# Optimization experiments

Hardware: AMD Instinct MI355X
Metric: run time of the kernel (lower is better)

## Reference

```python
import jax, jax.numpy as jnp
from jax import lax
import numpy as np

ANCHOR_LENGTHS = (2.0, 4.0, 6.0, 9.0, 13.0, 18.0)  # A = 6


def make_anchors_1d(Lf, anchor_lengths):
    # anchors on the feature axis: [Lf*A, 2] (start, end)
    al = jnp.asarray(anchor_lengths, dtype=jnp.float32)          # [A]
    centers = jnp.arange(Lf, dtype=jnp.float32) + 0.5            # [Lf]
    start = centers[:, None] - 0.5 * al[None, :]                 # [Lf, A]
    end = centers[:, None] + 0.5 * al[None, :]                   # [Lf, A]
    return jnp.stack([start, end], axis=-1).reshape(Lf * al.shape[0], 2)


def setup_inputs() -> dict:
    key = jax.random.key(0)
    ks = jax.random.split(key, 4)
    B, C, Lf, A = 4, 512, 8192, len(ANCHOR_LENGTHS)
    feat = jax.random.normal(ks[0], (B, C, Lf), dtype=jnp.float32)
    conv_w = jax.random.normal(ks[1], (C, C, 3), dtype=jnp.float32) * 0.02   # OIW
    conv_b = jnp.zeros((C,), dtype=jnp.float32)
    obj_w = jax.random.normal(ks[2], (A, C, 1), dtype=jnp.float32) * 0.02
    obj_b = jnp.zeros((A,), dtype=jnp.float32)
    reg_w = jax.random.normal(ks[3], (A * 2, C, 1), dtype=jnp.float32) * 0.02
    reg_b = jnp.zeros((A * 2,), dtype=jnp.float32)
    return {"feat": feat, "conv_w": conv_w, "conv_b": conv_b,
            "obj_w": obj_w, "obj_b": obj_b, "reg_w": reg_w, "reg_b": reg_b}


def reference(feat, conv_w, conv_b, obj_w, obj_b, reg_w, reg_b):
    B, C, Lf = feat.shape
    A = obj_w.shape[0]
    # 3x1 conv, padding=1 -> SAME; layout N C W / O I W
    h = lax.conv_general_dilated(feat, conv_w, window_strides=(1,),
                                 padding="SAME",
                                 dimension_numbers=("NCH", "OIH", "NCH"))
    h = jax.nn.relu(h + conv_b[None, :, None])                   # [B, C, Lf]
    # 1x1 conv heads expressed as channel contractions
    obj = jnp.einsum("bcl,ac->bal", h, obj_w[:, :, 0]) + obj_b[None, :, None]   # [B, A, Lf]
    reg = jnp.einsum("bcl,ac->bal", h, reg_w[:, :, 0]) + reg_b[None, :, None]   # [B, 2A, Lf]
    obj = obj.transpose(0, 2, 1).reshape(B, Lf * A)                              # [B, N]
    reg = reg.transpose(0, 2, 1).reshape(B, Lf, A, 2).reshape(B, Lf * A, 2)      # [B, N, 2]
    anchors = make_anchors_1d(Lf, ANCHOR_LENGTHS)                                # [N, 2]
    return obj, reg, anchors
```

## Files before the change

kernel.cpp:

```cpp
#include <hip/hip_runtime.h>
#include <stdint.h>

typedef __attribute__((ext_vector_type(8))) short short8;
typedef __attribute__((ext_vector_type(4))) float f32x4;
typedef __attribute__((ext_vector_type(4))) float float4v;
typedef __attribute__((ext_vector_type(4))) unsigned short u16x4;
typedef __attribute__((ext_vector_type(8))) unsigned short u16x8;

#define AS1 __attribute__((address_space(1)))
#define AS3 __attribute__((address_space(3)))


__device__ __forceinline__ unsigned short f2bf(float f) {
    union { float f; unsigned int u; } v; v.f = f;
    unsigned int r = v.u + 0x7fffu + ((v.u >> 16) & 1u);
    return (unsigned short)(r >> 16);
}

__constant__ float c_AL[6] = {2.f, 4.f, 6.f, 9.f, 13.f, 18.f};

__global__ __launch_bounds__(256) void prep_kernel(
    const float* __restrict__ conv_w, const float* __restrict__ obj_w,
    const float* __restrict__ reg_w, const float* __restrict__ obj_b,
    const float* __restrict__ reg_b, unsigned short* __restrict__ wAf,
    unsigned short* __restrict__ hwp, unsigned short* __restrict__ featT,
    float* __restrict__ out) {
    unsigned int idx = blockIdx.x * 256 + threadIdx.x;
    if (idx < 786432u) {
        unsigned int chunkid = idx >> 9;
        unsigned int within = idx & 511u;
        unsigned int lane = within >> 3, j = within & 7u;
        unsigned int kc = chunkid & 15u;
        unsigned int ct = chunkid >> 4;
        unsigned int t = ct % 3u, cb = ct / 3u;
        unsigned int cout = cb * 16u + (lane & 15u);
        unsigned int cin = kc * 32u + (lane >> 4) * 8u + j;
        wAf[idx] = f2bf(conv_w[(cout * 512u + cin) * 3u + t]);
    } else if (idx < 802816u) {
        unsigned int i2 = idx - 786432u;
        unsigned int j = i2 >> 9, c = i2 & 511u;
        float v = 0.f;
        if (j < 6u) v = obj_w[j * 512u + c];
        else if (j < 18u) v = reg_w[(j - 6u) * 512u + c];
        hwp[i2] = f2bf(v);
    } else if (idx < 851968u) {
        unsigned int n = idx - 802816u;
        unsigned int l = n / 6u, a = n - l * 6u;
        float ctr = (float)l + 0.5f, half = 0.5f * c_AL[a];
        float* anchors = out + 589824;
        anchors[2 * n]     = ctr - half;
        anchors[2 * n + 1] = ctr + half;
    } else if (idx < 856064u) {
        unsigned int i4 = idx - 851968u;
        unsigned int b = i4 >> 10, rem = i4 & 1023u;
        unsigned int row = (rem >> 9) ? 8193u : 0u;
        unsigned int c = rem & 511u;
        featT[((size_t)b * 8208 + row) * 512 + c] = 0;
    } else if (idx < 1052672u) {
        unsigned int i = idx - 856064u;
        out[i] = obj_b[i % 6u];
    } else if (idx < 1445888u) {
        unsigned int i = idx - 1052672u;
        out[196608u + i] = reg_b[i % 12u];
    }
}

__global__ __launch_bounds__(256) void transpose_kernel(
    const float* __restrict__ feat, unsigned short* __restrict__ featT) {
    __shared__ float tileT[64][69];
    int tid = threadIdx.x;
    int l0 = blockIdx.x * 64, c0 = blockIdx.y * 64, b = blockIdx.z;
    const float* fb = feat + ((size_t)b * 512 + c0) * 8192 + l0;
    #pragma unroll
    for (int it = 0; it < 4; ++it) {
        int slot = it * 256 + tid;
        int c = slot >> 4, l4 = (slot & 15) << 2;
        float4v v = *(const float4v*)(fb + (size_t)c * 8192 + l4);
        tileT[l4][c] = v.x; tileT[l4 + 1][c] = v.y;
        tileT[l4 + 2][c] = v.z; tileT[l4 + 3][c] = v.w;
    }
    __syncthreads();
    unsigned short* ftb = featT + ((size_t)b * 8208 + 1 + l0) * 512 + c0;
    #pragma unroll
    for (int it = 0; it < 2; ++it) {
        int slot = it * 256 + tid;
        int l = slot >> 3, c8 = (slot & 7) << 3;
        u16x8 pk;
        #pragma unroll
        for (int j = 0; j < 8; ++j) pk[j] = f2bf(tileT[l][c8 + j]);
        *(u16x8*)(ftb + (size_t)l * 512 + c8) = pk;
    }
}

__global__ __launch_bounds__(256, 3) void conv_gemm_kernel(
    const unsigned short* __restrict__ wAf,
    const unsigned short* __restrict__ featT,
    const float* __restrict__ conv_b,
    const unsigned short* __restrict__ hwp,
    float* __restrict__ out) {
    __shared__ unsigned short smem[17408];

    const int tid = threadIdx.x;
    const int wave = tid >> 6, lane = tid & 63;
    const int lq = lane >> 4, lr = lane & 15;
    const int l0 = blockIdx.x * 128;
    const int m0 = blockIdx.y * 128;
    const int b = blockIdx.z;
    const int wm = wave >> 1, wn = wave & 1;
    const unsigned short* ftb = featT + (size_t)b * 8208 * 512;

    f32x4 acc[4][4];
    #pragma unroll
    for (int i = 0; i < 4; ++i)
        #pragma unroll
        for (int j = 0; j < 4; ++j)
            acc[i][j] = (f32x4){0.f, 0.f, 0.f, 0.f};

    for (int kc = 0; kc < 16; ++kc) {
        __syncthreads();
        for (int ci = wave; ci < 33; ci += 4) {
            const unsigned short* g;
            if (ci < 24) {
                int t = ci >> 3, rb = ci & 7;
                g = wAf + ((size_t)(((m0 >> 4) + rb) * 3 + t) * 16 + kc) * 512 + lane * 8;
            } else {
                int lb = ci - 24;
                g = ftb + (size_t)(l0 + lb * 16 + lr) * 512 + kc * 32 + lq * 8;
            }
            __builtin_amdgcn_global_load_lds((const AS1 void*)g,
                                             (AS3 void*)(smem + ci * 512), 16, 0, 0);
        }
        __syncthreads();
        #pragma unroll
        for (int t = 0; t < 3; ++t) {
            short8 af[4], bf[4];
            #pragma unroll
            for (int fm = 0; fm < 4; ++fm)
                af[fm] = *(const short8*)(smem + ((t * 8 + wm * 4 + fm) << 9) + (lane << 3));
            #pragma unroll
            for (int fn = 0; fn < 4; ++fn) {
                int R = wn * 64 + fn * 16 + lr + t;
                bf[fn] = *(const short8*)(smem + ((24 + (R >> 4)) << 9) +
                                          ((((lq << 4) | (R & 15))) << 3));
            }
            #pragma unroll
            for (int fm = 0; fm < 4; ++fm)
                #pragma unroll
                for (int fn = 0; fn < 4; ++fn)
                    acc[fm][fn] = __builtin_amdgcn_mfma_f32_16x16x32_bf16(
                        af[fm], bf[fn], acc[fm][fn], 0, 0, 0);
        }
    }
    __syncthreads();
    #pragma unroll
    for (int fm = 0; fm < 4; ++fm) {
        int mb = wm * 64 + fm * 16 + lq * 4;
        float cb0 = conv_b[m0 + mb];
        float cb1 = conv_b[m0 + mb + 1];
        float cb2 = conv_b[m0 + mb + 2];
        float cb3 = conv_b[m0 + mb + 3];
        #pragma unroll
        for (int fn = 0; fn < 4; ++fn) {
            int n = wn * 64 + fn * 16 + lr;
            f32x4 v = acc[fm][fn];
            u16x4 pk;
            pk.x = f2bf(fmaxf(v.x + cb0, 0.f));
            pk.y = f2bf(fmaxf(v.y + cb1, 0.f));
            pk.z = f2bf(fmaxf(v.z + cb2, 0.f));
            pk.w = f2bf(fmaxf(v.w + cb3, 0.f));
            *(u16x4*)(smem + n * 136 + mb) = pk;
        }
    }
    __syncthreads();
    f32x4 hacc[2][2];
    #pragma unroll
    for (int i = 0; i < 2; ++i) {
        hacc[i][0] = (f32x4){0.f, 0.f, 0.f, 0.f};
        hacc[i][1] = (f32x4){0.f, 0.f, 0.f, 0.f};
    }
    const int lbase = wave * 32;
    for (int kk = 0; kk < 4; ++kk) {
        short8 ha[2], hb2[2];
        #pragma unroll
        for (int fm2 = 0; fm2 < 2; ++fm2)
            ha[fm2] = *(const short8*)(smem + (lbase + fm2 * 16 + lr) * 136 + kk * 32 + lq * 8);
        #pragma unroll
        for (int fn = 0; fn < 2; ++fn)
            hb2[fn] = *(const short8*)(hwp + (size_t)(fn * 16 + lr) * 512 + m0 + kk * 32 + lq * 8);
        #pragma unroll
        for (int fm2 = 0; fm2 < 2; ++fm2)
            #pragma unroll
            for (int fn = 0; fn < 2; ++fn)
                hacc[fm2][fn] = __builtin_amdgcn_mfma_f32_16x16x32_bf16(
                    ha[fm2], hb2[fn], hacc[fm2][fn], 0, 0, 0);
    }
    float* outObj = out + (size_t)b * 49152;
    float* outReg = out + 196608 + (size_t)b * 98304;
    #pragma unroll
    for (int fn = 0; fn < 2; ++fn) {
        int j = fn * 16 + lr;
        if (j >= 18) continue;
        #pragma unroll
        for (int fm2 = 0; fm2 < 2; ++fm2)
            #pragma unroll
            for (int r = 0; r < 4; ++r) {
                int l = l0 + lbase + fm2 * 16 + lq * 4 + r;
                float v = hacc[fm2][fn][r];
                if (j < 6) atomicAdd(&outObj[l * 6 + j], v);
                else atomicAdd(&outReg[l * 12 + (j - 6)], v);
            }
    }
}

extern "C" void kernel_launch(void* const* d_in, const int* in_sizes, int n_in,
                              void* d_out, int out_size, void* d_ws, size_t ws_size,
                              hipStream_t stream) {
    const float* feat   = (const float*)d_in[0];
    const float* conv_w = (const float*)d_in[1];
    const float* conv_b = (const float*)d_in[2];
    const float* obj_w  = (const float*)d_in[3];
    const float* obj_b  = (const float*)d_in[4];
    const float* reg_w  = (const float*)d_in[5];
    const float* reg_b  = (const float*)d_in[6];
    float* out = (float*)d_out;
    char* ws = (char*)d_ws;
    unsigned short* wAf   = (unsigned short*)(ws);
    unsigned short* hwp   = (unsigned short*)(ws + 1572864);
    unsigned short* featT = (unsigned short*)(ws + 1605632);

    prep_kernel<<<dim3(5648), dim3(256), 0, stream>>>(conv_w, obj_w, reg_w, obj_b,
                                                      reg_b, wAf, hwp, featT, out);
    transpose_kernel<<<dim3(128, 8, 4), dim3(256), 0, stream>>>(feat, featT);
    conv_gemm_kernel<<<dim3(64, 4, 4), dim3(256), 0, stream>>>(wAf, featT, conv_b, hwp, out);
}
```

Before: 176.6 us.

## Load conv weights directly to registers, replace head atomics with partial-sum reduce

The conv GEMM no longer stages weight fragments through LDS; each wave loads its A fragments straight from global memory into registers, and only the feature tile goes through LDS. The head outputs are written as per-channel-block partial sums into a workspace buffer, and a new reduce kernel adds the four partials plus biases, which replaces the float atomics and the bias pre-fill in prep. The transpose kernel converts to bf16 before staging, so its LDS tile holds 16-bit values. The trade-off is an extra kernel launch and partial-buffer traffic, and weight loads from global that are not shared across waves in the block.

```diff
diff --git a/kernel.cpp b/kernel.cpp
--- a/kernel.cpp
+++ b/kernel.cpp
@@ -21,8 +21,7 @@
 
 __global__ __launch_bounds__(256) void prep_kernel(
     const float* __restrict__ conv_w, const float* __restrict__ obj_w,
-    const float* __restrict__ reg_w, const float* __restrict__ obj_b,
-    const float* __restrict__ reg_b, unsigned short* __restrict__ wAf,
+    const float* __restrict__ reg_w, unsigned short* __restrict__ wAf,
     unsigned short* __restrict__ hwp, unsigned short* __restrict__ featT,
     float* __restrict__ out) {
     unsigned int idx = blockIdx.x * 256 + threadIdx.x;
@@ -56,18 +55,12 @@
         unsigned int row = (rem >> 9) ? 8193u : 0u;
         unsigned int c = rem & 511u;
         featT[((size_t)b * 8208 + row) * 512 + c] = 0;
-    } else if (idx < 1052672u) {
-        unsigned int i = idx - 856064u;
-        out[i] = obj_b[i % 6u];
-    } else if (idx < 1445888u) {
-        unsigned int i = idx - 1052672u;
-        out[196608u + i] = reg_b[i % 12u];
     }
 }
 
 __global__ __launch_bounds__(256) void transpose_kernel(
     const float* __restrict__ feat, unsigned short* __restrict__ featT) {
-    __shared__ float tileT[64][69];
+    __shared__ unsigned short tile[64][68];
     int tid = threadIdx.x;
     int l0 = blockIdx.x * 64, c0 = blockIdx.y * 64, b = blockIdx.z;
     const float* fb = feat + ((size_t)b * 512 + c0) * 8192 + l0;
@@ -76,8 +69,10 @@
         int slot = it * 256 + tid;
         int c = slot >> 4, l4 = (slot & 15) << 2;
         float4v v = *(const float4v*)(fb + (size_t)c * 8192 + l4);
-        tileT[l4][c] = v.x; tileT[l4 + 1][c] = v.y;
-        tileT[l4 + 2][c] = v.z; tileT[l4 + 3][c] = v.w;
+        u16x4 pk;
+        pk.x = f2bf(v.x); pk.y = f2bf(v.y);
+        pk.z = f2bf(v.z); pk.w = f2bf(v.w);
+        *(u16x4*)(&tile[c][l4]) = pk;
     }
     __syncthreads();
     unsigned short* ftb = featT + ((size_t)b * 8208 + 1 + l0) * 512 + c0;
@@ -87,7 +82,7 @@
         int l = slot >> 3, c8 = (slot & 7) << 3;
         u16x8 pk;
         #pragma unroll
-        for (int j = 0; j < 8; ++j) pk[j] = f2bf(tileT[l][c8 + j]);
+        for (int j = 0; j < 8; ++j) pk[j] = tile[c8 + j][l];
         *(u16x8*)(ftb + (size_t)l * 512 + c8) = pk;
     }
 }
@@ -97,7 +92,7 @@
     const unsigned short* __restrict__ featT,
     const float* __restrict__ conv_b,
     const unsigned short* __restrict__ hwp,
-    float* __restrict__ out) {
+    float* __restrict__ part) {
     __shared__ unsigned short smem[17408];
 
     const int tid = threadIdx.x;
@@ -118,29 +113,27 @@
 
     for (int kc = 0; kc < 16; ++kc) {
         __syncthreads();
-        for (int ci = wave; ci < 33; ci += 4) {
-            const unsigned short* g;
-            if (ci < 24) {
-                int t = ci >> 3, rb = ci & 7;
-                g = wAf + ((size_t)(((m0 >> 4) + rb) * 3 + t) * 16 + kc) * 512 + lane * 8;
-            } else {
-                int lb = ci - 24;
-                g = ftb + (size_t)(l0 + lb * 16 + lr) * 512 + kc * 32 + lq * 8;
-            }
+        for (int ci = wave; ci < 9; ci += 4) {
+            const unsigned short* g =
+                ftb + (size_t)(l0 + ci * 16 + lr) * 512 + kc * 32 + lq * 8;
             __builtin_amdgcn_global_load_lds((const AS1 void*)g,
                                              (AS3 void*)(smem + ci * 512), 16, 0, 0);
         }
+        short8 af[3][4];
+        #pragma unroll
+        for (int t = 0; t < 3; ++t)
+            #pragma unroll
+            for (int fm = 0; fm < 4; ++fm)
+                af[t][fm] = *(const short8*)(
+                    wAf + ((size_t)(((m0 >> 4) + wm * 4 + fm) * 3 + t) * 16 + kc) * 512 + lane * 8);
         __syncthreads();
         #pragma unroll
         for (int t = 0; t < 3; ++t) {
-            short8 af[4], bf[4];
-            #pragma unroll
-            for (int fm = 0; fm < 4; ++fm)
-                af[fm] = *(const short8*)(smem + ((t * 8 + wm * 4 + fm) << 9) + (lane << 3));
+            short8 bf[4];
             #pragma unroll
             for (int fn = 0; fn < 4; ++fn) {
                 int R = wn * 64 + fn * 16 + lr + t;
-                bf[fn] = *(const short8*)(smem + ((24 + (R >> 4)) << 9) +
+                bf[fn] = *(const short8*)(smem + ((R >> 4) << 9) +
                                           ((((lq << 4) | (R & 15))) << 3));
             }
             #pragma unroll
@@ -148,7 +141,7 @@
                 #pragma unroll
                 for (int fn = 0; fn < 4; ++fn)
                     acc[fm][fn] = __builtin_amdgcn_mfma_f32_16x16x32_bf16(
-                        af[fm], bf[fn], acc[fm][fn], 0, 0, 0);
+                        af[t][fm], bf[fn], acc[fm][fn], 0, 0, 0);
         }
     }
     __syncthreads();
@@ -194,8 +187,7 @@
                 hacc[fm2][fn] = __builtin_amdgcn_mfma_f32_16x16x32_bf16(
                     ha[fm2], hb2[fn], hacc[fm2][fn], 0, 0, 0);
     }
-    float* outObj = out + (size_t)b * 49152;
-    float* outReg = out + 196608 + (size_t)b * 98304;
+    float* pb = part + ((size_t)(blockIdx.y * 4 + b) * 8192) * 18;
     #pragma unroll
     for (int fn = 0; fn < 2; ++fn) {
         int j = fn * 16 + lr;
@@ -205,10 +197,30 @@
             #pragma unroll
             for (int r = 0; r < 4; ++r) {
                 int l = l0 + lbase + fm2 * 16 + lq * 4 + r;
-                float v = hacc[fm2][fn][r];
-                if (j < 6) atomicAdd(&outObj[l * 6 + j], v);
-                else atomicAdd(&outReg[l * 12 + (j - 6)], v);
+                pb[(size_t)l * 18 + j] = hacc[fm2][fn][r];
             }
+    }
+}
+
+__global__ __launch_bounds__(256) void reduce_kernel(
+    const float* __restrict__ part, const float* __restrict__ obj_b,
+    const float* __restrict__ reg_b, float* __restrict__ out) {
+    unsigned int idx = blockIdx.x * 256 + threadIdx.x;
+    if (idx >= 589824u) return;
+    unsigned int j = idx % 18u;
+    unsigned int t = idx / 18u;
+    unsigned int l = t & 8191u;
+    unsigned int b = t >> 13;
+    float s = 0.f;
+    #pragma unroll
+    for (int mb = 0; mb < 4; ++mb)
+        s += part[((size_t)(mb * 4 + b) * 8192 + l) * 18 + j];
+    if (j < 6u) {
+        s += obj_b[j];
+        out[(size_t)b * 49152 + l * 6 + j] = s;
+    } else {
+        s += reg_b[j - 6u];
+        out[196608u + (size_t)b * 98304 + l * 12 + (j - 6u)] = s;
     }
 }
 
@@ -227,9 +239,11 @@
     unsigned short* wAf   = (unsigned short*)(ws);
     unsigned short* hwp   = (unsigned short*)(ws + 1572864);
     unsigned short* featT = (unsigned short*)(ws + 1605632);
-
-    prep_kernel<<<dim3(5648), dim3(256), 0, stream>>>(conv_w, obj_w, reg_w, obj_b,
-                                                      reg_b, wAf, hwp, featT, out);
+    float* part           = (float*)(ws + 35225600);
+
+    prep_kernel<<<dim3(3344), dim3(256), 0, stream>>>(conv_w, obj_w, reg_w,
+                                                      wAf, hwp, featT, out);
     transpose_kernel<<<dim3(128, 8, 4), dim3(256), 0, stream>>>(feat, featT);
-    conv_gemm_kernel<<<dim3(64, 4, 4), dim3(256), 0, stream>>>(wAf, featT, conv_b, hwp, out);
-}
+    conv_gemm_kernel<<<dim3(64, 4, 4), dim3(256), 0, stream>>>(wAf, featT, conv_b, hwp, part);
+    reduce_kernel<<<dim3(2304), dim3(256), 0, stream>>>(part, obj_b, reg_b, out);
+}
```

Result: no change. 174.6 us (-1.2%).
